# Kernel optimization log

Hardware: AMD Instinct MI355X
Metric: run time of the kernel (lower is better)

## Reference

```python
import jax, jax.numpy as jnp
import numpy as np

B, T, C = 64, 384, 256
NH, NKV = 4, 2
HD = C // NH            # 64
NREP = NH // NKV        # 2
NE, TOPK = 8, 2
HID = int(8 / 3 * C)    # 682
EPS_RMS = 1e-6


def _rope_tables(t_len):
    inv_freq = 1.0 / (10000.0 ** (np.arange(0, HD, 2, dtype=np.float32) / HD))
    t = np.arange(t_len, dtype=np.float32)
    freqs = np.outer(t, inv_freq)                      # [T, HD/2]
    emb = np.concatenate([freqs, freqs], axis=-1)      # [T, HD]
    return jnp.asarray(np.cos(emb)), jnp.asarray(np.sin(emb))


def _rotate_half(x):
    h = x.shape[-1] // 2
    return jnp.concatenate([-x[..., h:], x[..., :h]], axis=-1)


def _rmsnorm(v, w):
    return v * jax.lax.rsqrt(jnp.mean(v * v, axis=-1, keepdims=True) + EPS_RMS) * w


def setup_inputs() -> dict:
    key = jax.random.key(0)
    ks = jax.random.split(key, 10)
    s = lambda k, shape: (jax.random.normal(k, shape, jnp.float32) * 0.02)
    return {
        "x": jax.random.normal(ks[0], (B, T, C), jnp.float32),
        "ln1_w": jnp.ones((C,), jnp.float32),
        "ln2_w": jnp.ones((C,), jnp.float32),
        "wq": s(ks[1], (NH * HD, C)),
        "wk": s(ks[2], (NKV * HD, C)),
        "wv": s(ks[3], (NKV * HD, C)),
        "wo": s(ks[4], (C, C)),
        "router_w": s(ks[5], (NE, C)),
        "w1": s(ks[6], (NE, HID, C)),
        "w2": s(ks[7], (NE, C, HID)),
        "w3": s(ks[8], (NE, HID, C)),
    }


def reference(x, ln1_w, ln2_w, wq, wk, wv, wo, router_w, w1, w2, w3):
    Bx, Tx, Cx = x.shape
    # --- attention sub-block ---
    h = _rmsnorm(x, ln1_w)
    q = (h @ wq.T).reshape(Bx, Tx, NH, HD).transpose(0, 2, 1, 3)    # [B,H,T,D]
    k = (h @ wk.T).reshape(Bx, Tx, NKV, HD).transpose(0, 2, 1, 3)   # [B,KV,T,D]
    v = (h @ wv.T).reshape(Bx, Tx, NKV, HD).transpose(0, 2, 1, 3)
    cos, sin = _rope_tables(Tx)
    cos, sin = cos[None, None], sin[None, None]
    q = q * cos + _rotate_half(q) * sin
    k = k * cos + _rotate_half(k) * sin
    k = jnp.repeat(k, NREP, axis=1)   # GQA: expand kv heads
    v = jnp.repeat(v, NREP, axis=1)
    scores = jnp.einsum('bhtd,bhsd->bhts', q, k) / jnp.sqrt(jnp.float32(HD))
    causal = jnp.tril(jnp.ones((Tx, Tx), dtype=bool))
    scores = jnp.where(causal[None, None], scores, jnp.float32(-1e30))
    att = jax.nn.softmax(scores, axis=-1)
    y = jnp.einsum('bhts,bhsd->bhtd', att, v).transpose(0, 2, 1, 3).reshape(Bx, Tx, Cx)
    x = x + y @ wo.T

    # --- MoE sub-block ---
    flat = _rmsnorm(x, ln2_w).reshape(-1, Cx)                  # [N, C]
    probs = jax.nn.softmax(flat @ router_w.T, axis=-1)         # [N, NE]
    tp, ti = jax.lax.top_k(probs, TOPK)
    tp = tp / (jnp.sum(tp, axis=-1, keepdims=True) + 1e-9)
    # per-token per-expert combine weight (0 if not selected)
    weights = jnp.sum(tp[..., None] * jax.nn.one_hot(ti, NE, dtype=flat.dtype), axis=1)  # [N, NE]
    out = jnp.zeros_like(flat)
    for e in range(NE):  # small fixed expert count
        hh = jax.nn.silu(flat @ w1[e].T) * (flat @ w3[e].T)
        out = out + weights[:, e:e + 1] * (hh @ w2[e].T)
    return x + out.reshape(Bx, Tx, Cx)
```

## Files before the change

### kernel.cpp

```cpp
#include <hip/hip_runtime.h>
#include <hip/hip_bf16.h>
#include <math.h>

typedef unsigned short u16t;
typedef __bf16 bf16x8 __attribute__((ext_vector_type(8)));
typedef float f32x4 __attribute__((ext_vector_type(4)));

#define NBATCH 64
#define NT 384
#define NC 256
#define NHID 682
#define NHIDP 704
#define NTOK (NBATCH * NT)
#define NSLOT (2 * NTOK + 1024)

#define SB0 196
#define SB1 (SB0 + 512)
#define SB2 (SB1 + 256)
#define SB3 (SB2 + 5632)
#define SB4 (SB3 + 5632)
#define SB5 (SB4 + 48)

static __device__ __forceinline__ float bf2f(u16t u) { return __uint_as_float(((unsigned int)u) << 16); }
static __device__ __forceinline__ u16t f2bf(float f) { return __builtin_bit_cast(u16t, __float2bfloat16(f)); }

static __device__ __forceinline__ void gload16(const void* gp, void* lp) {
  __builtin_amdgcn_global_load_lds((const __attribute__((address_space(1))) void*)gp,
                                   (__attribute__((address_space(3))) void*)lp, 16, 0, 0);
}


__global__ __launch_bounds__(256) void k_setup(const float* __restrict__ wq, const float* __restrict__ wk,
                                               const float* __restrict__ wv, const float* __restrict__ wo,
                                               const float* __restrict__ w1, const float* __restrict__ w2,
                                               const float* __restrict__ w3,
                                               int* __restrict__ tok, float* __restrict__ tokw,
                                               int* __restrict__ ctrl,
                                               u16t* __restrict__ wqkvb, u16t* __restrict__ wob,
                                               u16t* __restrict__ w1p, u16t* __restrict__ w3p,
                                               u16t* __restrict__ w2p, float* __restrict__ rtab) {
  int blk = blockIdx.x, t = threadIdx.x;
  if (blk < SB0) {
    int i = blk * 256 + t;
    tok[i] = -1; tokw[i] = 0.f;
    if (blk == 0 && t < 64) ctrl[t] = 0;
  } else if (blk < SB1) {
    int i = (blk - SB0) * 256 + t;
    int row = i >> 8, col = i & 255;
    float s = (row < 256) ? wq[(size_t)row * 256 + col]
            : (row < 384) ? wk[(size_t)(row - 256) * 256 + col]
                          : wv[(size_t)(row - 384) * 256 + col];
    wqkvb[i] = f2bf(s);
  } else if (blk < SB2) {
    int i = (blk - SB1) * 256 + t;
    wob[i] = f2bf(wo[i]);
  } else if (blk < SB3) {
    int idx = (blk - SB2) * 256 + t;
    int kcol = idx & 255; int tmp = idx >> 8; int nrow = tmp % NHIDP; int e = tmp / NHIDP;
    if (nrow < NHID) {
      size_t src = ((size_t)e * NHID + nrow) * NC + kcol;
      w1p[idx] = f2bf(w1[src]); w3p[idx] = f2bf(w3[src]);
    } else { w1p[idx] = 0; w3p[idx] = 0; }
  } else if (blk < SB4) {
    int idx = (blk - SB3) * 256 + t;
    int kcol = idx % NHIDP; int tmp = idx / NHIDP; int nrow = tmp & 255; int e = tmp >> 8;
    w2p[idx] = (kcol < NHID) ? f2bf(w2[((size_t)e * NC + nrow) * NHID + kcol]) : (u16t)0;
  } else {
    int i = (blk - SB4) * 256 + t;
    int tt = i >> 5, d = i & 31;
    float ang = (float)tt * powf(10000.f, -(float)d * (1.f / 32.f));
    float s, c; sincosf(ang, &s, &c);
    ((float2*)rtab)[i] = make_float2(c, s);
  }
}

__global__ __launch_bounds__(256) void k_rms(const float* __restrict__ xin,
                                             const float* __restrict__ wg,
                                             u16t* __restrict__ out) {
  int w = threadIdx.x >> 6, l = threadIdx.x & 63;
  int n = blockIdx.x * 4 + w;
  const float* xr = xin + (size_t)n * NC;
  float4 xa = *(const float4*)(xr + l * 4);
  float ssq = xa.x * xa.x + xa.y * xa.y + xa.z * xa.z + xa.w * xa.w;
  for (int d = 1; d < 64; d <<= 1) ssq += __shfl_xor(ssq, d, 64);
  float rs = rsqrtf(ssq * (1.f / 256.f) + 1e-6f);
  float4 wa = *(const float4*)(wg + l * 4);
  ushort4 o;
  o.x = f2bf(xa.x * rs * wa.x);
  o.y = f2bf(xa.y * rs * wa.y);
  o.z = f2bf(xa.z * rs * wa.z);
  o.w = f2bf(xa.w * rs * wa.w);
  *(ushort4*)(out + (size_t)n * NC + l * 4) = o;
}

__global__ __launch_bounds__(256) void k_rms_router(const float* __restrict__ xin,
                                                    const float* __restrict__ wg,
                                                    const float* __restrict__ rw,
                                                    u16t* __restrict__ flat,
                                                    int* __restrict__ eidx,
                                                    float* __restrict__ ew) {
  int w = threadIdx.x >> 6, l = threadIdx.x & 63;
  int n = blockIdx.x * 4 + w;
  const float* xr = xin + (size_t)n * NC;
  float4 xa = *(const float4*)(xr + l * 4);
  float ssq = xa.x * xa.x + xa.y * xa.y + xa.z * xa.z + xa.w * xa.w;
  for (int d = 1; d < 64; d <<= 1) ssq += __shfl_xor(ssq, d, 64);
  float rs = rsqrtf(ssq * (1.f / 256.f) + 1e-6f);
  float4 wa = *(const float4*)(wg + l * 4);
  float n0 = xa.x * rs * wa.x, n1 = xa.y * rs * wa.y;
  float n2 = xa.z * rs * wa.z, n3 = xa.w * rs * wa.w;
  ushort4 o; o.x = f2bf(n0); o.y = f2bf(n1); o.z = f2bf(n2); o.w = f2bf(n3);
  *(ushort4*)(flat + (size_t)n * NC + l * 4) = o;
  float acc[8];
  for (int e = 0; e < 8; e++) {
    float4 ra = *(const float4*)(rw + (size_t)e * NC + l * 4);
    acc[e] = n0 * ra.x + n1 * ra.y + n2 * ra.z + n3 * ra.w;
  }
  for (int e = 0; e < 8; e++)
    for (int d = 1; d < 64; d <<= 1) acc[e] += __shfl_xor(acc[e], d, 64);
  if (l == 0) {
    float mx = acc[0];
    for (int e = 1; e < 8; e++) mx = fmaxf(mx, acc[e]);
    float p[8], sum = 0.f;
    for (int e = 0; e < 8; e++) { p[e] = __expf(acc[e] - mx); sum += p[e]; }
    float inv = 1.f / sum;
    for (int e = 0; e < 8; e++) p[e] *= inv;
    int i0 = 0; float b0 = p[0];
    for (int e = 1; e < 8; e++) if (p[e] > b0) { b0 = p[e]; i0 = e; }
    int i1 = -1; float b1 = -1.f;
    for (int e = 0; e < 8; e++) if (e != i0 && p[e] > b1) { b1 = p[e]; i1 = e; }
    float s2 = 1.f / (b0 + b1 + 1e-9f);
    eidx[n * 2] = i0; eidx[n * 2 + 1] = i1;
    ew[n * 2] = b0 * s2; ew[n * 2 + 1] = b1 * s2;
  }
}

__global__ __launch_bounds__(256) void k_hist(const int* __restrict__ eidx, int* __restrict__ ctrl) {
  int* cnt = ctrl; int* offs = ctrl + 8; int* cursor = ctrl + 20; int* done = ctrl + 32;
  __shared__ int lh[8];
  if (threadIdx.x < 8) lh[threadIdx.x] = 0;
  __syncthreads();
  int base = blockIdx.x * 1024 + threadIdx.x;
  for (int i = 0; i < 4; i++) atomicAdd(&lh[eidx[base + i * 256]], 1);
  __syncthreads();
  if (threadIdx.x < 8) {
    atomicAdd(&cnt[threadIdx.x], lh[threadIdx.x]);
    __threadfence();
  }
  __syncthreads();
  if (threadIdx.x == 0) {
    int prev = atomicAdd(done, 1);
    if (prev == 47) {
      int off = 0;
      for (int e = 0; e < 8; e++) {
        int c_ = atomicAdd(&cnt[e], 0);
        offs[e] = off; cursor[e] = off;
        off += ((c_ + 127) >> 7) << 7;
      }
      offs[8] = off;
    }
  }
}

__global__ __launch_bounds__(256) void k_gemm_qkv(const u16t* __restrict__ A,
                                                  const u16t* __restrict__ Bw,
                                                  const float* __restrict__ rtab,
                                                  u16t* __restrict__ qkv) {
  __shared__ __align__(16) u16t sA[128 * 64];
  __shared__ __align__(16) u16t sB[128 * 64];
  int t = threadIdx.x;
  int m0 = blockIdx.y * 128, n0 = blockIdx.x * 128;
  int w = t >> 6, l = t & 63, quad = l >> 4, lq = l & 15;
  int wm = (w >> 1) * 64, wn = (w & 1) * 64;
  const u16t* aP[4]; const u16t* bP[4];
  for (int i = 0; i < 4; i++) {
    int c = i * 256 + t; int r = c >> 3; int g = (c & 7) ^ (r & 7);
    aP[i] = A + (size_t)(m0 + r) * NC + g * 8;
    bP[i] = Bw + (size_t)(n0 + r) * NC + g * 8;
  }
  const f32x4 fz = {0.f, 0.f, 0.f, 0.f};
  f32x4 acc[4][4];
  for (int i = 0; i < 4; i++) for (int j = 0; j < 4; j++) acc[i][j] = fz;
  for (int kb = 0; kb < 4; kb++) {
    int k0 = kb << 6;
    for (int i = 0; i < 4; i++) {
      gload16(aP[i] + k0, sA + (size_t)(i * 256 + t) * 8);
      gload16(bP[i] + k0, sB + (size_t)(i * 256 + t) * 8);
    }
    __syncthreads();
    for (int kk = 0; kk < 2; kk++) {
      int gq = kk * 4 + quad;
      bf16x8 af[4], bf[4];
      for (int mi = 0; mi < 4; mi++) { int row = wm + mi * 16 + lq; af[mi] = *(const bf16x8*)(sA + (row * 8 + (gq ^ (row & 7))) * 8); }
      for (int ni = 0; ni < 4; ni++) { int row = wn + ni * 16 + lq; bf[ni] = *(const bf16x8*)(sB + (row * 8 + (gq ^ (row & 7))) * 8); }
      for (int mi = 0; mi < 4; mi++)
        for (int ni = 0; ni < 4; ni++)
          acc[mi][ni] = __builtin_amdgcn_mfma_f32_16x16x32_bf16(af[mi], bf[ni], acc[mi][ni], 0, 0, 0);
    }
    __syncthreads();
  }
  int cb = (n0 + wn) >> 6;
  const float2* rt = (const float2*)rtab;
  for (int mi = 0; mi < 4; mi++)
    for (int r = 0; r < 4; r++) {
      int gm = m0 + wm + mi * 16 + quad * 4 + r;
      u16t* orow = qkv + (size_t)gm * 512 + n0 + wn;
      if (cb < 6) {
        int tt = gm % NT;
        for (int ni = 0; ni < 2; ni++) {
          int d = ni * 16 + lq;
          float2 cs = rt[tt * 32 + d];
          float x1 = acc[mi][ni][r], x2 = acc[mi][ni + 2][r];
          orow[d] = f2bf(x1 * cs.x - x2 * cs.y);
          orow[d + 32] = f2bf(x2 * cs.x + x1 * cs.y);
        }
      } else {
        for (int ni = 0; ni < 4; ni++) orow[ni * 16 + lq] = f2bf(acc[mi][ni][r]);
      }
    }
}

__global__ __launch_bounds__(256) void k_gemm_wo(const u16t* __restrict__ A,
                                                 const u16t* __restrict__ Bw,
                                                 const float* __restrict__ xin,
                                                 float* __restrict__ xo) {
  __shared__ __align__(16) u16t sA[128 * 64];
  __shared__ __align__(16) u16t sB[128 * 64];
  int t = threadIdx.x;
  int m0 = blockIdx.y * 128, n0 = blockIdx.x * 128;
  int w = t >> 6, l = t & 63, quad = l >> 4, lq = l & 15;
  int wm = (w >> 1) * 64, wn = (w & 1) * 64;
  const u16t* aP[4]; const u16t* bP[4];
  for (int i = 0; i < 4; i++) {
    int c = i * 256 + t; int r = c >> 3; int g = (c & 7) ^ (r & 7);
    aP[i] = A + (size_t)(m0 + r) * NC + g * 8;
    bP[i] = Bw + (size_t)(n0 + r) * NC + g * 8;
  }
  const f32x4 fz = {0.f, 0.f, 0.f, 0.f};
  f32x4 acc[4][4];
  for (int i = 0; i < 4; i++) for (int j = 0; j < 4; j++) acc[i][j] = fz;
  for (int kb = 0; kb < 4; kb++) {
    int k0 = kb << 6;
    for (int i = 0; i < 4; i++) {
      gload16(aP[i] + k0, sA + (size_t)(i * 256 + t) * 8);
      gload16(bP[i] + k0, sB + (size_t)(i * 256 + t) * 8);
    }
    __syncthreads();
    for (int kk = 0; kk < 2; kk++) {
      int gq = kk * 4 + quad;
      bf16x8 af[4], bf[4];
      for (int mi = 0; mi < 4; mi++) { int row = wm + mi * 16 + lq; af[mi] = *(const bf16x8*)(sA + (row * 8 + (gq ^ (row & 7))) * 8); }
      for (int ni = 0; ni < 4; ni++) { int row = wn + ni * 16 + lq; bf[ni] = *(const bf16x8*)(sB + (row * 8 + (gq ^ (row & 7))) * 8); }
      for (int mi = 0; mi < 4; mi++)
        for (int ni = 0; ni < 4; ni++)
          acc[mi][ni] = __builtin_amdgcn_mfma_f32_16x16x32_bf16(af[mi], bf[ni], acc[mi][ni], 0, 0, 0);
    }
    __syncthreads();
  }
  for (int mi = 0; mi < 4; mi++)
    for (int ni = 0; ni < 4; ni++) {
      int gn = n0 + wn + ni * 16 + lq;
      for (int r = 0; r < 4; r++) {
        int gm = m0 + wm + mi * 16 + quad * 4 + r;
        xo[(size_t)gm * NC + gn] = acc[mi][ni][r] + xin[(size_t)gm * NC + gn];
      }
    }
}

__global__ __launch_bounds__(256) void k_attn(const u16t* __restrict__ qkv,
                                              u16t* __restrict__ y) {
  __shared__ __align__(16) u16t sK[64 * 64];
  __shared__ __align__(16) u16t sVT[64 * 64];
  __shared__ __align__(16) u16t sP[4 * 32 * 64];
  int qt = blockIdx.x, h = blockIdx.y, b = blockIdx.z;
  int kvh = h >> 1;
  int t = threadIdx.x, w = t >> 6, l = t & 63, quad = l >> 4, lq = l & 15;
  int tb = qt * 128 + w * 32;
  bf16x8 qf[2][2];
  for (int mi = 0; mi < 2; mi++)
    for (int kk = 0; kk < 2; kk++)
      qf[mi][kk] = *(const bf16x8*)(qkv + ((size_t)(b * NT + tb + mi * 16 + lq)) * 512 + h * 64 + kk * 32 + quad * 8);
  const f32x4 fz = {0.f, 0.f, 0.f, 0.f};
  f32x4 accO[2][4];
  float mrow[2][4], lrow[2][4];
  for (int mi = 0; mi < 2; mi++)
    for (int ni = 0; ni < 4; ni++) accO[mi][ni] = fz;
  for (int mi = 0; mi < 2; mi++)
    for (int r = 0; r < 4; r++) { mrow[mi][r] = -1e30f; lrow[mi][r] = 0.f; }
  u16t* myP = sP + w * 2048;
  int nkt = (qt + 1) * 2;
  for (int kt = 0; kt < nkt; kt++) {
    int s0 = kt * 64;
    for (int i = 0; i < 2; i++) {
      int c = i * 256 + t; int s = c >> 3; int g = (c & 7) ^ (s & 7);
      gload16(qkv + ((size_t)(b * NT + s0 + s)) * 512 + 256 + kvh * 64 + g * 8, sK + (size_t)c * 8);
    }
    for (int i = 0; i < 2; i++) {
      int p = i * 256 + t; int n0g = p >> 6; int s = p & 63; int n0 = n0g * 8;
      const u16t* vp = qkv + ((size_t)(b * NT + s0 + s)) * 512 + 384 + kvh * 64 + n0;
      ushort4 v0 = *(const ushort4*)vp; ushort4 v1 = *(const ushort4*)(vp + 4);
      u16t vv[8] = {v0.x, v0.y, v0.z, v0.w, v1.x, v1.y, v1.z, v1.w};
      for (int j = 0; j < 8; j++) {
        int nn = n0 + j;
        sVT[(nn * 8 + ((s >> 3) ^ (nn & 7))) * 8 + (s & 7)] = vv[j];
      }
    }
    __syncthreads();
    if (s0 <= tb + 31) {
      f32x4 accS[2][4];
      for (int mi = 0; mi < 2; mi++) for (int ni = 0; ni < 4; ni++) accS[mi][ni] = fz;
      for (int kk = 0; kk < 2; kk++) {
        int gq = kk * 4 + quad;
        bf16x8 kf[4];
        for (int ni = 0; ni < 4; ni++) { int row = ni * 16 + lq; kf[ni] = *(const bf16x8*)(sK + (row * 8 + (gq ^ (row & 7))) * 8); }
        for (int mi = 0; mi < 2; mi++)
          for (int ni = 0; ni < 4; ni++)
            accS[mi][ni] = __builtin_amdgcn_mfma_f32_16x16x32_bf16(qf[mi][kk], kf[ni], accS[mi][ni], 0, 0, 0);
      }
      for (int mi = 0; mi < 2; mi++) {
        float alpha[4];
        for (int r = 0; r < 4; r++) {
          int trow = tb + mi * 16 + quad * 4 + r;
          float mx = -1e30f;
          for (int ni = 0; ni < 4; ni++) {
            int ss = s0 + ni * 16 + lq;
            float sv = accS[mi][ni][r] * 0.125f;
            sv = (ss > trow) ? -1e30f : sv;
            accS[mi][ni][r] = sv;
            mx = fmaxf(mx, sv);
          }
          for (int d = 1; d < 16; d <<= 1) mx = fmaxf(mx, __shfl_xor(mx, d, 64));
          float mnew = fmaxf(mrow[mi][r], mx);
          float al = __expf(mrow[mi][r] - mnew);
          float rsum = 0.f;
          for (int ni = 0; ni < 4; ni++) {
            float p = __expf(accS[mi][ni][r] - mnew);
            accS[mi][ni][r] = p;
            rsum += p;
          }
          for (int d = 1; d < 16; d <<= 1) rsum += __shfl_xor(rsum, d, 64);
          lrow[mi][r] = lrow[mi][r] * al + rsum;
          mrow[mi][r] = mnew;
          alpha[r] = al;
        }
        for (int ni = 0; ni < 4; ni++)
          for (int r = 0; r < 4; r++) accO[mi][ni][r] *= alpha[r];
        for (int ni = 0; ni < 4; ni++) {
          int cc = ni * 16 + lq;
          for (int r = 0; r < 4; r++) {
            int row = mi * 16 + quad * 4 + r;
            myP[((cc >> 3) * 32 + row) * 8 + (cc & 7)] = f2bf(accS[mi][ni][r]);
          }
        }
      }
      asm volatile("s_waitcnt lgkmcnt(0)" ::: "memory");
      for (int kk = 0; kk < 2; kk++) {
        int gq = kk * 4 + quad;
        bf16x8 pf[2], vf[4];
        for (int mi = 0; mi < 2; mi++) { int row = mi * 16 + lq; pf[mi] = *(const bf16x8*)(myP + (gq * 32 + row) * 8); }
        for (int ni = 0; ni < 4; ni++) { int row = ni * 16 + lq; vf[ni] = *(const bf16x8*)(sVT + (row * 8 + (gq ^ (row & 7))) * 8); }
        for (int mi = 0; mi < 2; mi++)
          for (int ni = 0; ni < 4; ni++)
            accO[mi][ni] = __builtin_amdgcn_mfma_f32_16x16x32_bf16(pf[mi], vf[ni], accO[mi][ni], 0, 0, 0);
      }
    }
    __syncthreads();
  }
  for (int mi = 0; mi < 2; mi++)
    for (int r = 0; r < 4; r++) {
      int trow = tb + mi * 16 + quad * 4 + r;
      float inv = 1.f / lrow[mi][r];
      for (int ni = 0; ni < 4; ni++) {
        int d = ni * 16 + lq;
        y[((size_t)(b * NT + trow)) * NC + h * 64 + d] = f2bf(accO[mi][ni][r] * inv);
      }
    }
}

__global__ __launch_bounds__(256) void k_scatter(const int* __restrict__ eidx, const float* __restrict__ ew,
                                                 int* __restrict__ cursor, int* __restrict__ tok,
                                                 float* __restrict__ tokw, int* __restrict__ t2s) {
  __shared__ int lcnt[8], lbase[8];
  if (threadIdx.x < 8) lcnt[threadIdx.x] = 0;
  __syncthreads();
  int n = blockIdx.x * 256 + threadIdx.x;
  int e0 = eidx[n * 2], e1 = eidx[n * 2 + 1];
  int p0 = atomicAdd(&lcnt[e0], 1);
  int p1 = atomicAdd(&lcnt[e1], 1);
  __syncthreads();
  if (threadIdx.x < 8) lbase[threadIdx.x] = atomicAdd(&cursor[threadIdx.x], lcnt[threadIdx.x]);
  __syncthreads();
  int g0 = lbase[e0] + p0, g1 = lbase[e1] + p1;
  tok[g0] = n; tokw[g0] = ew[n * 2];
  tok[g1] = n; tokw[g1] = ew[n * 2 + 1];
  t2s[n * 2] = g0; t2s[n * 2 + 1] = g1;
}

__global__ __launch_bounds__(256) void k_moe_e1(const u16t* __restrict__ flat,
                                                const u16t* __restrict__ w1p,
                                                const u16t* __restrict__ w3p,
                                                const int* __restrict__ offs,
                                                const int* __restrict__ tok,
                                                u16t* __restrict__ hh) {
  __shared__ __align__(16) u16t sA[128 * 64];
  __shared__ __align__(16) u16t sB1[64 * 64];
  __shared__ __align__(16) u16t sB3[64 * 64];
  int t = threadIdx.x;
  int bid = blockIdx.x;
  int work = (bid & 7) * 539 + (bid >> 3);
  int sb = work / 11;
  int slot0 = sb * 128, n0 = (work - sb * 11) * 64;
  int e = 7;
  for (int i = 0; i < 8; i++) { if (slot0 < offs[i + 1]) { e = i; break; } }
  const u16t* B1 = w1p + (size_t)e * NHIDP * NC;
  const u16t* B3 = w3p + (size_t)e * NHIDP * NC;
  int w = t >> 6, l = t & 63, quad = l >> 4, lq = l & 15;
  int wm = (w >> 1) * 64, wn = (w & 1) * 32;
  const u16t* aP[4]; const u16t* b1P[2]; const u16t* b3P[2];
  for (int i = 0; i < 4; i++) {
    int c = i * 256 + t; int r = c >> 3; int g = (c & 7) ^ (r & 7);
    int tk = tok[slot0 + r]; int row = (tk < 0) ? 0 : tk;
    aP[i] = flat + (size_t)row * NC + g * 8;
  }
  for (int i = 0; i < 2; i++) {
    int c = i * 256 + t; int r = c >> 3; int g = (c & 7) ^ (r & 7);
    b1P[i] = B1 + (size_t)(n0 + r) * NC + g * 8;
    b3P[i] = B3 + (size_t)(n0 + r) * NC + g * 8;
  }
  const f32x4 fz = {0.f, 0.f, 0.f, 0.f};
  f32x4 a1[4][2], a3[4][2];
  for (int i = 0; i < 4; i++) for (int j = 0; j < 2; j++) { a1[i][j] = fz; a3[i][j] = fz; }
  for (int kb = 0; kb < 4; kb++) {
    int k0 = kb << 6;
    for (int i = 0; i < 4; i++)
      gload16(aP[i] + k0, sA + (size_t)(i * 256 + t) * 8);
    for (int i = 0; i < 2; i++) {
      gload16(b1P[i] + k0, sB1 + (size_t)(i * 256 + t) * 8);
      gload16(b3P[i] + k0, sB3 + (size_t)(i * 256 + t) * 8);
    }
    __syncthreads();
    for (int kk = 0; kk < 2; kk++) {
      int gq = kk * 4 + quad;
      bf16x8 af[4], b1f[2], b3f[2];
      for (int mi = 0; mi < 4; mi++) { int row = wm + mi * 16 + lq; af[mi] = *(const bf16x8*)(sA + (row * 8 + (gq ^ (row & 7))) * 8); }
      for (int ni = 0; ni < 2; ni++) {
        int row = wn + ni * 16 + lq;
        b1f[ni] = *(const bf16x8*)(sB1 + (row * 8 + (gq ^ (row & 7))) * 8);
        b3f[ni] = *(const bf16x8*)(sB3 + (row * 8 + (gq ^ (row & 7))) * 8);
      }
      for (int mi = 0; mi < 4; mi++)
        for (int ni = 0; ni < 2; ni++) {
          a1[mi][ni] = __builtin_amdgcn_mfma_f32_16x16x32_bf16(af[mi], b1f[ni], a1[mi][ni], 0, 0, 0);
          a3[mi][ni] = __builtin_amdgcn_mfma_f32_16x16x32_bf16(af[mi], b3f[ni], a3[mi][ni], 0, 0, 0);
        }
    }
    __syncthreads();
  }
  for (int mi = 0; mi < 4; mi++)
    for (int ni = 0; ni < 2; ni++) {
      int gn = n0 + wn + ni * 16 + lq;
      for (int r = 0; r < 4; r++) {
        int slot = slot0 + wm + mi * 16 + quad * 4 + r;
        float v1 = a1[mi][ni][r], v3 = a3[mi][ni][r];
        float hv = v1 / (1.f + __expf(-v1)) * v3;
        hh[(size_t)slot * NHIDP + gn] = f2bf(hv);
      }
    }
}

__global__ __launch_bounds__(256) void k_moe_e2(const u16t* __restrict__ hh,
                                                const u16t* __restrict__ w2p,
                                                const int* __restrict__ offs,
                                                const float* __restrict__ tokw,
                                                u16t* __restrict__ eo) {
  __shared__ __align__(16) u16t sA[128 * 64];
  __shared__ __align__(16) u16t sB[128 * 64];
  int t = threadIdx.x;
  int bid = blockIdx.x;
  int work = (bid & 7) * 98 + (bid >> 3);
  int slot0 = (work >> 1) * 128, n0 = (work & 1) * 128;
  int e = 7;
  for (int i = 0; i < 8; i++) { if (slot0 < offs[i + 1]) { e = i; break; } }
  const u16t* Bw = w2p + (size_t)e * NC * NHIDP;
  int w = t >> 6, l = t & 63, quad = l >> 4, lq = l & 15;
  int wm = (w >> 1) * 64, wn = (w & 1) * 64;
  const u16t* aP[4]; const u16t* bP[4];
  for (int i = 0; i < 4; i++) {
    int c = i * 256 + t; int r = c >> 3; int g = (c & 7) ^ (r & 7);
    aP[i] = hh + (size_t)(slot0 + r) * NHIDP + g * 8;
    bP[i] = Bw + (size_t)(n0 + r) * NHIDP + g * 8;
  }
  const f32x4 fz = {0.f, 0.f, 0.f, 0.f};
  f32x4 acc[4][4];
  for (int i = 0; i < 4; i++) for (int j = 0; j < 4; j++) acc[i][j] = fz;
  for (int kb = 0; kb < 11; kb++) {
    int k0 = kb << 6;
    for (int i = 0; i < 4; i++) {
      gload16(aP[i] + k0, sA + (size_t)(i * 256 + t) * 8);
      gload16(bP[i] + k0, sB + (size_t)(i * 256 + t) * 8);
    }
    __syncthreads();
    for (int kk = 0; kk < 2; kk++) {
      int gq = kk * 4 + quad;
      bf16x8 af[4], bf[4];
      for (int mi = 0; mi < 4; mi++) { int row = wm + mi * 16 + lq; af[mi] = *(const bf16x8*)(sA + (row * 8 + (gq ^ (row & 7))) * 8); }
      for (int ni = 0; ni < 4; ni++) { int row = wn + ni * 16 + lq; bf[ni] = *(const bf16x8*)(sB + (row * 8 + (gq ^ (row & 7))) * 8); }
      for (int mi = 0; mi < 4; mi++)
        for (int ni = 0; ni < 4; ni++)
          acc[mi][ni] = __builtin_amdgcn_mfma_f32_16x16x32_bf16(af[mi], bf[ni], acc[mi][ni], 0, 0, 0);
    }
    __syncthreads();
  }
  for (int mi = 0; mi < 4; mi++)
    for (int r = 0; r < 4; r++) {
      int slot = slot0 + wm + mi * 16 + quad * 4 + r;
      float wgt = tokw[slot];
      for (int ni = 0; ni < 4; ni++) {
        int gn = n0 + wn + ni * 16 + lq;
        eo[(size_t)slot * NC + gn] = f2bf(wgt * acc[mi][ni][r]);
      }
    }
}

__global__ __launch_bounds__(256) void k_combine(const u16t* __restrict__ eo,
                                                 const int* __restrict__ t2s,
                                                 float* __restrict__ xo) {
  int w = threadIdx.x >> 6, l = threadIdx.x & 63;
  int n = blockIdx.x * 4 + w;
  int g0 = t2s[n * 2], g1 = t2s[n * 2 + 1];
  float* xr = xo + (size_t)n * NC + l * 4;
  float4 xa = *(const float4*)xr;
  ushort4 a = *(const ushort4*)(eo + (size_t)g0 * NC + l * 4);
  ushort4 b = *(const ushort4*)(eo + (size_t)g1 * NC + l * 4);
  xa.x += bf2f(a.x) + bf2f(b.x);
  xa.y += bf2f(a.y) + bf2f(b.y);
  xa.z += bf2f(a.z) + bf2f(b.z);
  xa.w += bf2f(a.w) + bf2f(b.w);
  *(float4*)xr = xa;
}

extern "C" void kernel_launch(void* const* d_in, const int* in_sizes, int n_in,
                              void* d_out, int out_size, void* d_ws, size_t ws_size,
                              hipStream_t stream) {
  (void)in_sizes; (void)n_in; (void)out_size; (void)ws_size;
  const float* x    = (const float*)d_in[0];
  const float* ln1w = (const float*)d_in[1];
  const float* ln2w = (const float*)d_in[2];
  const float* wq   = (const float*)d_in[3];
  const float* wk   = (const float*)d_in[4];
  const float* wv   = (const float*)d_in[5];
  const float* wo   = (const float*)d_in[6];
  const float* rw   = (const float*)d_in[7];
  const float* w1   = (const float*)d_in[8];
  const float* w2   = (const float*)d_in[9];
  const float* w3   = (const float*)d_in[10];
  float* xo = (float*)d_out;

  char* ws = (char*)d_ws;
  size_t off = 0;
  int* ctrl  = (int*)(ws + off);  off += 4096;
  int* eidx  = (int*)(ws + off);  off += (size_t)NTOK * 2 * 4;
  float* ew  = (float*)(ws + off); off += (size_t)NTOK * 2 * 4;
  int* tok   = (int*)(ws + off);  off += (size_t)NSLOT * 4;
  float* tokw = (float*)(ws + off); off += (size_t)NSLOT * 4;
  int* t2s   = (int*)(ws + off);  off += (size_t)NTOK * 2 * 4;
  u16t* wqkvb = (u16t*)(ws + off); off += (size_t)512 * 256 * 2;
  u16t* wob  = (u16t*)(ws + off); off += (size_t)256 * 256 * 2;
  u16t* w1p  = (u16t*)(ws + off); off += (size_t)8 * NHIDP * NC * 2;
  u16t* w3p  = (u16t*)(ws + off); off += (size_t)8 * NHIDP * NC * 2;
  u16t* w2p  = (u16t*)(ws + off); off += (size_t)8 * NC * NHIDP * 2;
  float* rtab = (float*)(ws + off); off += (size_t)NT * 32 * 2 * 4;
  u16t* h    = (u16t*)(ws + off); off += (size_t)NTOK * NC * 2;
  u16t* qkv  = (u16t*)(ws + off); off += (size_t)NTOK * 512 * 2;
  u16t* y    = (u16t*)(ws + off); off += (size_t)NTOK * NC * 2;
  u16t* flat = (u16t*)(ws + off); off += (size_t)NTOK * NC * 2;
  u16t* hh   = (u16t*)(ws + off); off += (size_t)NSLOT * NHIDP * 2;
  u16t* eo   = h;
  int* offs = ctrl + 8; int* cursor = ctrl + 20;

  k_setup<<<SB5, 256, 0, stream>>>(wq, wk, wv, wo, w1, w2, w3,
                                   tok, tokw, ctrl, wqkvb, wob, w1p, w3p, w2p, rtab);
  k_rms<<<NTOK / 4, 256, 0, stream>>>(x, ln1w, h);
  k_gemm_qkv<<<dim3(4, NTOK / 128), 256, 0, stream>>>(h, wqkvb, rtab, qkv);
  k_attn<<<dim3(3, 4, NBATCH), 256, 0, stream>>>(qkv, y);
  k_gemm_wo<<<dim3(2, NTOK / 128), 256, 0, stream>>>(y, wob, x, xo);

  k_rms_router<<<NTOK / 4, 256, 0, stream>>>(xo, ln2w, rw, flat, eidx, ew);
  k_hist<<<48, 256, 0, stream>>>(eidx, ctrl);
  k_scatter<<<NTOK / 256, 256, 0, stream>>>(eidx, ew, cursor, tok, tokw, t2s);
  k_moe_e1<<<4312, 256, 0, stream>>>(flat, w1p, w3p, offs, tok, hh);
  k_moe_e2<<<784, 256, 0, stream>>>(hh, w2p, offs, tokw, eo);
  k_combine<<<NTOK / 4, 256, 0, stream>>>(eo, t2s, xo);
}
```

Baseline: 312.2 us.

## Double-buffer LDS tiles across GEMM and attention kernels

Converts the GEMM kernels (qkv, wo, MoE expert up/down) and the attention kernel to double-buffered shared memory, so each next K tile is loaded while the current tile feeds the MFMAs. A single wait-and-barrier per iteration replaces the two __syncthreads. Attention now holds V in registers and writes it to LDS after compute. This doubles LDS use per block, which may lower occupancy, and the full vmcnt(0) wait still limits how much load latency is hidden.

```diff
diff --git a/kernel.cpp b/kernel.cpp
--- a/kernel.cpp
+++ b/kernel.cpp
@@ -27,6 +27,12 @@
 static __device__ __forceinline__ void gload16(const void* gp, void* lp) {
   __builtin_amdgcn_global_load_lds((const __attribute__((address_space(1))) void*)gp,
                                    (__attribute__((address_space(3))) void*)lp, 16, 0, 0);
+}
+
+static __device__ __forceinline__ void pipe_barrier_full() {
+  asm volatile("s_waitcnt vmcnt(0) lgkmcnt(0)" ::: "memory");
+  __builtin_amdgcn_s_barrier();
+  asm volatile("" ::: "memory");
 }
 
 
@@ -166,8 +172,8 @@
                                                   const u16t* __restrict__ Bw,
                                                   const float* __restrict__ rtab,
                                                   u16t* __restrict__ qkv) {
-  __shared__ __align__(16) u16t sA[128 * 64];
-  __shared__ __align__(16) u16t sB[128 * 64];
+  __shared__ __align__(16) u16t sA[2][128 * 64];
+  __shared__ __align__(16) u16t sB[2][128 * 64];
   int t = threadIdx.x;
   int m0 = blockIdx.y * 128, n0 = blockIdx.x * 128;
   int w = t >> 6, l = t & 63, quad = l >> 4, lq = l & 15;
@@ -178,26 +184,30 @@
     aP[i] = A + (size_t)(m0 + r) * NC + g * 8;
     bP[i] = Bw + (size_t)(n0 + r) * NC + g * 8;
   }
+  auto stage = [&](int p, int k0) {
+    for (int i = 0; i < 4; i++) {
+      gload16(aP[i] + k0, sA[p] + (size_t)(i * 256 + t) * 8);
+      gload16(bP[i] + k0, sB[p] + (size_t)(i * 256 + t) * 8);
+    }
+  };
   const f32x4 fz = {0.f, 0.f, 0.f, 0.f};
   f32x4 acc[4][4];
   for (int i = 0; i < 4; i++) for (int j = 0; j < 4; j++) acc[i][j] = fz;
+  stage(0, 0);
+  pipe_barrier_full();
   for (int kb = 0; kb < 4; kb++) {
-    int k0 = kb << 6;
-    for (int i = 0; i < 4; i++) {
-      gload16(aP[i] + k0, sA + (size_t)(i * 256 + t) * 8);
-      gload16(bP[i] + k0, sB + (size_t)(i * 256 + t) * 8);
-    }
-    __syncthreads();
+    int p = kb & 1;
+    if (kb < 3) stage(p ^ 1, (kb + 1) << 6);
     for (int kk = 0; kk < 2; kk++) {
       int gq = kk * 4 + quad;
       bf16x8 af[4], bf[4];
-      for (int mi = 0; mi < 4; mi++) { int row = wm + mi * 16 + lq; af[mi] = *(const bf16x8*)(sA + (row * 8 + (gq ^ (row & 7))) * 8); }
-      for (int ni = 0; ni < 4; ni++) { int row = wn + ni * 16 + lq; bf[ni] = *(const bf16x8*)(sB + (row * 8 + (gq ^ (row & 7))) * 8); }
+      for (int mi = 0; mi < 4; mi++) { int row = wm + mi * 16 + lq; af[mi] = *(const bf16x8*)(sA[p] + (row * 8 + (gq ^ (row & 7))) * 8); }
+      for (int ni = 0; ni < 4; ni++) { int row = wn + ni * 16 + lq; bf[ni] = *(const bf16x8*)(sB[p] + (row * 8 + (gq ^ (row & 7))) * 8); }
       for (int mi = 0; mi < 4; mi++)
         for (int ni = 0; ni < 4; ni++)
           acc[mi][ni] = __builtin_amdgcn_mfma_f32_16x16x32_bf16(af[mi], bf[ni], acc[mi][ni], 0, 0, 0);
     }
-    __syncthreads();
+    if (kb < 3) pipe_barrier_full();
   }
   int cb = (n0 + wn) >> 6;
   const float2* rt = (const float2*)rtab;
@@ -224,8 +234,8 @@
                                                  const u16t* __restrict__ Bw,
                                                  const float* __restrict__ xin,
                                                  float* __restrict__ xo) {
-  __shared__ __align__(16) u16t sA[128 * 64];
-  __shared__ __align__(16) u16t sB[128 * 64];
+  __shared__ __align__(16) u16t sA[2][128 * 64];
+  __shared__ __align__(16) u16t sB[2][128 * 64];
   int t = threadIdx.x;
   int m0 = blockIdx.y * 128, n0 = blockIdx.x * 128;
   int w = t >> 6, l = t & 63, quad = l >> 4, lq = l & 15;
@@ -236,26 +246,30 @@
     aP[i] = A + (size_t)(m0 + r) * NC + g * 8;
     bP[i] = Bw + (size_t)(n0 + r) * NC + g * 8;
   }
+  auto stage = [&](int p, int k0) {
+    for (int i = 0; i < 4; i++) {
+      gload16(aP[i] + k0, sA[p] + (size_t)(i * 256 + t) * 8);
+      gload16(bP[i] + k0, sB[p] + (size_t)(i * 256 + t) * 8);
+    }
+  };
   const f32x4 fz = {0.f, 0.f, 0.f, 0.f};
   f32x4 acc[4][4];
   for (int i = 0; i < 4; i++) for (int j = 0; j < 4; j++) acc[i][j] = fz;
+  stage(0, 0);
+  pipe_barrier_full();
   for (int kb = 0; kb < 4; kb++) {
-    int k0 = kb << 6;
-    for (int i = 0; i < 4; i++) {
-      gload16(aP[i] + k0, sA + (size_t)(i * 256 + t) * 8);
-      gload16(bP[i] + k0, sB + (size_t)(i * 256 + t) * 8);
-    }
-    __syncthreads();
+    int p = kb & 1;
+    if (kb < 3) stage(p ^ 1, (kb + 1) << 6);
     for (int kk = 0; kk < 2; kk++) {
       int gq = kk * 4 + quad;
       bf16x8 af[4], bf[4];
-      for (int mi = 0; mi < 4; mi++) { int row = wm + mi * 16 + lq; af[mi] = *(const bf16x8*)(sA + (row * 8 + (gq ^ (row & 7))) * 8); }
-      for (int ni = 0; ni < 4; ni++) { int row = wn + ni * 16 + lq; bf[ni] = *(const bf16x8*)(sB + (row * 8 + (gq ^ (row & 7))) * 8); }
+      for (int mi = 0; mi < 4; mi++) { int row = wm + mi * 16 + lq; af[mi] = *(const bf16x8*)(sA[p] + (row * 8 + (gq ^ (row & 7))) * 8); }
+      for (int ni = 0; ni < 4; ni++) { int row = wn + ni * 16 + lq; bf[ni] = *(const bf16x8*)(sB[p] + (row * 8 + (gq ^ (row & 7))) * 8); }
       for (int mi = 0; mi < 4; mi++)
         for (int ni = 0; ni < 4; ni++)
           acc[mi][ni] = __builtin_amdgcn_mfma_f32_16x16x32_bf16(af[mi], bf[ni], acc[mi][ni], 0, 0, 0);
     }
-    __syncthreads();
+    if (kb < 3) pipe_barrier_full();
   }
   for (int mi = 0; mi < 4; mi++)
     for (int ni = 0; ni < 4; ni++) {
@@ -269,8 +283,8 @@
 
 __global__ __launch_bounds__(256) void k_attn(const u16t* __restrict__ qkv,
                                               u16t* __restrict__ y) {
-  __shared__ __align__(16) u16t sK[64 * 64];
-  __shared__ __align__(16) u16t sVT[64 * 64];
+  __shared__ __align__(16) u16t sK[2][64 * 64];
+  __shared__ __align__(16) u16t sVT[2][64 * 64];
   __shared__ __align__(16) u16t sP[4 * 32 * 64];
   int qt = blockIdx.x, h = blockIdx.y, b = blockIdx.z;
   int kvh = h >> 1;
@@ -289,30 +303,46 @@
     for (int r = 0; r < 4; r++) { mrow[mi][r] = -1e30f; lrow[mi][r] = 0.f; }
   u16t* myP = sP + w * 2048;
   int nkt = (qt + 1) * 2;
-  for (int kt = 0; kt < nkt; kt++) {
+  ushort4 vr0[2], vr1[2];
+  auto stageK = [&](int p, int kt) {
     int s0 = kt * 64;
     for (int i = 0; i < 2; i++) {
       int c = i * 256 + t; int s = c >> 3; int g = (c & 7) ^ (s & 7);
-      gload16(qkv + ((size_t)(b * NT + s0 + s)) * 512 + 256 + kvh * 64 + g * 8, sK + (size_t)c * 8);
-    }
+      gload16(qkv + ((size_t)(b * NT + s0 + s)) * 512 + 256 + kvh * 64 + g * 8, sK[p] + (size_t)c * 8);
+    }
+  };
+  auto vload = [&](int kt) {
+    int s0 = kt * 64;
     for (int i = 0; i < 2; i++) {
-      int p = i * 256 + t; int n0g = p >> 6; int s = p & 63; int n0 = n0g * 8;
+      int pI = i * 256 + t; int s = pI & 63; int n0 = (pI >> 6) * 8;
       const u16t* vp = qkv + ((size_t)(b * NT + s0 + s)) * 512 + 384 + kvh * 64 + n0;
-      ushort4 v0 = *(const ushort4*)vp; ushort4 v1 = *(const ushort4*)(vp + 4);
-      u16t vv[8] = {v0.x, v0.y, v0.z, v0.w, v1.x, v1.y, v1.z, v1.w};
+      vr0[i] = *(const ushort4*)vp; vr1[i] = *(const ushort4*)(vp + 4);
+    }
+  };
+  auto vstore = [&](int p) {
+    for (int i = 0; i < 2; i++) {
+      int pI = i * 256 + t; int s = pI & 63; int n0 = (pI >> 6) * 8;
+      u16t vv[8] = {vr0[i].x, vr0[i].y, vr0[i].z, vr0[i].w, vr1[i].x, vr1[i].y, vr1[i].z, vr1[i].w};
       for (int j = 0; j < 8; j++) {
         int nn = n0 + j;
-        sVT[(nn * 8 + ((s >> 3) ^ (nn & 7))) * 8 + (s & 7)] = vv[j];
-      }
-    }
-    __syncthreads();
+        sVT[p][(nn * 8 + ((s >> 3) ^ (nn & 7))) * 8 + (s & 7)] = vv[j];
+      }
+    }
+  };
+  stageK(0, 0); vload(0); vstore(0);
+  pipe_barrier_full();
+  for (int kt = 0; kt < nkt; kt++) {
+    int p = kt & 1;
+    int s0 = kt * 64;
+    bool more = (kt + 1 < nkt);
+    if (more) { stageK(p ^ 1, kt + 1); vload(kt + 1); }
     if (s0 <= tb + 31) {
       f32x4 accS[2][4];
       for (int mi = 0; mi < 2; mi++) for (int ni = 0; ni < 4; ni++) accS[mi][ni] = fz;
       for (int kk = 0; kk < 2; kk++) {
         int gq = kk * 4 + quad;
         bf16x8 kf[4];
-        for (int ni = 0; ni < 4; ni++) { int row = ni * 16 + lq; kf[ni] = *(const bf16x8*)(sK + (row * 8 + (gq ^ (row & 7))) * 8); }
+        for (int ni = 0; ni < 4; ni++) { int row = ni * 16 + lq; kf[ni] = *(const bf16x8*)(sK[p] + (row * 8 + (gq ^ (row & 7))) * 8); }
         for (int mi = 0; mi < 2; mi++)
           for (int ni = 0; ni < 4; ni++)
             accS[mi][ni] = __builtin_amdgcn_mfma_f32_16x16x32_bf16(qf[mi][kk], kf[ni], accS[mi][ni], 0, 0, 0);
@@ -334,9 +364,9 @@
           float al = __expf(mrow[mi][r] - mnew);
           float rsum = 0.f;
           for (int ni = 0; ni < 4; ni++) {
-            float p = __expf(accS[mi][ni][r] - mnew);
-            accS[mi][ni][r] = p;
-            rsum += p;
+            float p2 = __expf(accS[mi][ni][r] - mnew);
+            accS[mi][ni][r] = p2;
+            rsum += p2;
           }
           for (int d = 1; d < 16; d <<= 1) rsum += __shfl_xor(rsum, d, 64);
           lrow[mi][r] = lrow[mi][r] * al + rsum;
@@ -358,13 +388,16 @@
         int gq = kk * 4 + quad;
         bf16x8 pf[2], vf[4];
         for (int mi = 0; mi < 2; mi++) { int row = mi * 16 + lq; pf[mi] = *(const bf16x8*)(myP + (gq * 32 + row) * 8); }
-        for (int ni = 0; ni < 4; ni++) { int row = ni * 16 + lq; vf[ni] = *(const bf16x8*)(sVT + (row * 8 + (gq ^ (row & 7))) * 8); }
+        for (int ni = 0; ni < 4; ni++) { int row = ni * 16 + lq; vf[ni] = *(const bf16x8*)(sVT[p] + (row * 8 + (gq ^ (row & 7))) * 8); }
         for (int mi = 0; mi < 2; mi++)
           for (int ni = 0; ni < 4; ni++)
             accO[mi][ni] = __builtin_amdgcn_mfma_f32_16x16x32_bf16(pf[mi], vf[ni], accO[mi][ni], 0, 0, 0);
       }
     }
-    __syncthreads();
+    if (more) {
+      vstore(p ^ 1);
+      pipe_barrier_full();
+    }
   }
   for (int mi = 0; mi < 2; mi++)
     for (int r = 0; r < 4; r++) {
@@ -402,9 +435,9 @@
                                                 const int* __restrict__ offs,
                                                 const int* __restrict__ tok,
                                                 u16t* __restrict__ hh) {
-  __shared__ __align__(16) u16t sA[128 * 64];
-  __shared__ __align__(16) u16t sB1[64 * 64];
-  __shared__ __align__(16) u16t sB3[64 * 64];
+  __shared__ __align__(16) u16t sA[2][128 * 64];
+  __shared__ __align__(16) u16t sB1[2][64 * 64];
+  __shared__ __align__(16) u16t sB3[2][64 * 64];
   int t = threadIdx.x;
   int bid = blockIdx.x;
   int work = (bid & 7) * 539 + (bid >> 3);
@@ -427,26 +460,30 @@
     b1P[i] = B1 + (size_t)(n0 + r) * NC + g * 8;
     b3P[i] = B3 + (size_t)(n0 + r) * NC + g * 8;
   }
+  auto stage = [&](int p, int k0) {
+    for (int i = 0; i < 4; i++)
+      gload16(aP[i] + k0, sA[p] + (size_t)(i * 256 + t) * 8);
+    for (int i = 0; i < 2; i++) {
+      gload16(b1P[i] + k0, sB1[p] + (size_t)(i * 256 + t) * 8);
+      gload16(b3P[i] + k0, sB3[p] + (size_t)(i * 256 + t) * 8);
+    }
+  };
   const f32x4 fz = {0.f, 0.f, 0.f, 0.f};
   f32x4 a1[4][2], a3[4][2];
   for (int i = 0; i < 4; i++) for (int j = 0; j < 2; j++) { a1[i][j] = fz; a3[i][j] = fz; }
+  stage(0, 0);
+  pipe_barrier_full();
   for (int kb = 0; kb < 4; kb++) {
-    int k0 = kb << 6;
-    for (int i = 0; i < 4; i++)
-      gload16(aP[i] + k0, sA + (size_t)(i * 256 + t) * 8);
-    for (int i = 0; i < 2; i++) {
-      gload16(b1P[i] + k0, sB1 + (size_t)(i * 256 + t) * 8);
-      gload16(b3P[i] + k0, sB3 + (size_t)(i * 256 + t) * 8);
-    }
-    __syncthreads();
+    int p = kb & 1;
+    if (kb < 3) stage(p ^ 1, (kb + 1) << 6);
     for (int kk = 0; kk < 2; kk++) {
       int gq = kk * 4 + quad;
       bf16x8 af[4], b1f[2], b3f[2];
-      for (int mi = 0; mi < 4; mi++) { int row = wm + mi * 16 + lq; af[mi] = *(const bf16x8*)(sA + (row * 8 + (gq ^ (row & 7))) * 8); }
+      for (int mi = 0; mi < 4; mi++) { int row = wm + mi * 16 + lq; af[mi] = *(const bf16x8*)(sA[p] + (row * 8 + (gq ^ (row & 7))) * 8); }
       for (int ni = 0; ni < 2; ni++) {
         int row = wn + ni * 16 + lq;
-        b1f[ni] = *(const bf16x8*)(sB1 + (row * 8 + (gq ^ (row & 7))) * 8);
-        b3f[ni] = *(const bf16x8*)(sB3 + (row * 8 + (gq ^ (row & 7))) * 8);
+        b1f[ni] = *(const bf16x8*)(sB1[p] + (row * 8 + (gq ^ (row & 7))) * 8);
+        b3f[ni] = *(const bf16x8*)(sB3[p] + (row * 8 + (gq ^ (row & 7))) * 8);
       }
       for (int mi = 0; mi < 4; mi++)
         for (int ni = 0; ni < 2; ni++) {
@@ -454,7 +491,7 @@
           a3[mi][ni] = __builtin_amdgcn_mfma_f32_16x16x32_bf16(af[mi], b3f[ni], a3[mi][ni], 0, 0, 0);
         }
     }
-    __syncthreads();
+    if (kb < 3) pipe_barrier_full();
   }
   for (int mi = 0; mi < 4; mi++)
     for (int ni = 0; ni < 2; ni++) {
@@ -473,8 +510,8 @@
                                                 const int* __restrict__ offs,
                                                 const float* __restrict__ tokw,
                                                 u16t* __restrict__ eo) {
-  __shared__ __align__(16) u16t sA[128 * 64];
-  __shared__ __align__(16) u16t sB[128 * 64];
+  __shared__ __align__(16) u16t sA[2][128 * 64];
+  __shared__ __align__(16) u16t sB[2][128 * 64];
   int t = threadIdx.x;
   int bid = blockIdx.x;
   int work = (bid & 7) * 98 + (bid >> 3);
@@ -490,26 +527,30 @@
     aP[i] = hh + (size_t)(slot0 + r) * NHIDP + g * 8;
     bP[i] = Bw + (size_t)(n0 + r) * NHIDP + g * 8;
   }
+  auto stage = [&](int p, int k0) {
+    for (int i = 0; i < 4; i++) {
+      gload16(aP[i] + k0, sA[p] + (size_t)(i * 256 + t) * 8);
+      gload16(bP[i] + k0, sB[p] + (size_t)(i * 256 + t) * 8);
+    }
+  };
   const f32x4 fz = {0.f, 0.f, 0.f, 0.f};
   f32x4 acc[4][4];
   for (int i = 0; i < 4; i++) for (int j = 0; j < 4; j++) acc[i][j] = fz;
+  stage(0, 0);
+  pipe_barrier_full();
   for (int kb = 0; kb < 11; kb++) {
-    int k0 = kb << 6;
-    for (int i = 0; i < 4; i++) {
-      gload16(aP[i] + k0, sA + (size_t)(i * 256 + t) * 8);
-      gload16(bP[i] + k0, sB + (size_t)(i * 256 + t) * 8);
-    }
-    __syncthreads();
+    int p = kb & 1;
+    if (kb < 10) stage(p ^ 1, (kb + 1) << 6);
     for (int kk = 0; kk < 2; kk++) {
       int gq = kk * 4 + quad;
       bf16x8 af[4], bf[4];
-      for (int mi = 0; mi < 4; mi++) { int row = wm + mi * 16 + lq; af[mi] = *(const bf16x8*)(sA + (row * 8 + (gq ^ (row & 7))) * 8); }
-      for (int ni = 0; ni < 4; ni++) { int row = wn + ni * 16 + lq; bf[ni] = *(const bf16x8*)(sB + (row * 8 + (gq ^ (row & 7))) * 8); }
+      for (int mi = 0; mi < 4; mi++) { int row = wm + mi * 16 + lq; af[mi] = *(const bf16x8*)(sA[p] + (row * 8 + (gq ^ (row & 7))) * 8); }
+      for (int ni = 0; ni < 4; ni++) { int row = wn + ni * 16 + lq; bf[ni] = *(const bf16x8*)(sB[p] + (row * 8 + (gq ^ (row & 7))) * 8); }
       for (int mi = 0; mi < 4; mi++)
         for (int ni = 0; ni < 4; ni++)
           acc[mi][ni] = __builtin_amdgcn_mfma_f32_16x16x32_bf16(af[mi], bf[ni], acc[mi][ni], 0, 0, 0);
     }
-    __syncthreads();
+    if (kb < 10) pipe_barrier_full();
   }
   for (int mi = 0; mi < 4; mi++)
     for (int r = 0; r < 4; r++) {
```

New measurement: 306.7 us. Within noise of the previous version (-1.8%).
